# Performance work log

Hardware: AMD Instinct MI355X
Metric: run time of the kernel (lower is better)

## Reference

```python
import jax, jax.numpy as jnp
import numpy as np

FS = 48000
RIR_LENGTH = 96000
FILTER_LENGTH = 1023          # odd, so hilbert_one_sided works: N = 2*F - 1
N_FREQ = (FILTER_LENGTH + 1) // 2   # 512 rfft bins
SHARPNESS = 8.0
EPS = 1e-9
# strictly increasing fit-frequency bin indices (10 bands, like surface_freqs/dir_freqs)
FREQ_IDX = np.array([1, 2, 4, 8, 16, 32, 64, 128, 256, 480])


def get_interpolator(n_freq_target, fi):
    """numpy port of the torch get_interpolator (precomputed constant)."""
    fi = np.asarray(fi)
    r = np.zeros((len(fi), n_freq_target), np.float32)
    d = np.diff(fi)
    for i in range(len(fi)):
        if i == 0:
            r[0, :fi[1]] = np.concatenate([np.ones(fi[0]), 1 - np.arange(d[0]) / d[0]])
        elif i == len(fi) - 1:
            r[i, fi[i - 1]:] = np.concatenate([np.arange(d[i - 1]) / d[i - 1], np.ones(n_freq_target - fi[i])])
        else:
            r[i, fi[i - 1]:fi[i + 1]] = np.concatenate([np.arange(d[i - 1]) / d[i - 1], 1 - np.arange(d[i]) / d[i]])
    return r


def fibonacci_sphere(n):
    i = np.arange(n, dtype=np.float64)
    phi = np.pi * (np.sqrt(5.0) - 1.0)
    y = 1 - i / (n - 1) * 2
    rad = np.sqrt(np.maximum(1 - y * y, 0.0))
    th = phi * i
    return np.stack([np.cos(th) * rad, y, np.sin(th) * rad], -1).astype(np.float32)


def safe_log(x):
    return jnp.log(jnp.where(x <= EPS, EPS, x))


def hilbert_one_sided(x):
    """Minimum phase from log-magnitude. x: [..., F] with N = 2F-1 odd."""
    F = x.shape[-1]
    N = 2 * F - 1
    Xf = jnp.fft.irfft(x, n=N, axis=-1)
    h = jnp.concatenate([jnp.ones((1,), x.dtype),
                         2.0 * jnp.ones(((N + 1) // 2 - 1,), x.dtype),
                         jnp.zeros((N - (N + 1) // 2,), x.dtype)])
    return jnp.imag(jnp.fft.rfft(Xf * h, axis=-1))


def setup_inputs() -> dict:
    key = jax.random.key(0)
    ks = jax.random.split(key, 6)
    B, P, S, NF = 8, 4096, 16, 128
    interp = get_interpolator(N_FREQ, FREQ_IDX)  # [10, 512]
    return {
        "surface_params": jax.random.normal(ks[0], (S, len(FREQ_IDX)), jnp.float32),
        "dir_params": jax.random.normal(ks[1], (NF, len(FREQ_IDX)), jnp.float32),
        "path_dirs": jax.random.normal(ks[2], (B, P, 3), jnp.float32),
        "source_kernel": jax.random.normal(ks[3], (FILTER_LENGTH,), jnp.float32) * 0.02,
        "surf_interp": jnp.asarray(interp),
        "dir_interp": jnp.asarray(interp),
        "fib_points": jnp.asarray(fibonacci_sphere(NF)),
        "mask": jax.random.randint(ks[4], (B, P, S), 0, 3, jnp.int32),
        "delays": jax.random.randint(ks[5], (B, P), 100, RIR_LENGTH - FILTER_LENGTH - 1, jnp.int32),
    }


def reference(surface_params, dir_params, path_dirs, source_kernel,
              surf_interp, dir_interp, fib_points, mask, delays):
    B, P, _ = path_dirs.shape
    # --- per-path surface reflection log-magnitude at fit frequencies ---
    log_refl = safe_log(jax.nn.sigmoid(surface_params))            # [S, Fs]
    log_amp_s = jnp.einsum('bps,sf->bpf', mask.astype(jnp.float32), log_refl)  # [B,P,Fs]
    # --- source directivity via fibonacci-sphere softmax weighting ---
    d = path_dirs / (jnp.linalg.norm(path_dirs, axis=-1, keepdims=True) + EPS)
    w = jax.nn.softmax(SHARPNESS * jnp.einsum('bpc,nc->bpn', d, fib_points), axis=-1)  # [B,P,N]
    log_amp_d = safe_log(jnp.einsum('bpn,nf->bpf', w, jax.nn.sigmoid(dir_params)))     # [B,P,Fd]
    # --- interpolate to full frequency grid (precomputed linterp matmuls) ---
    log_amp = (jnp.einsum('bpf,fq->bpq', log_amp_s, surf_interp) +
               jnp.einsum('bpf,fq->bpq', log_amp_d, dir_interp))   # [B,P,512]
    # --- minimum phase + irfft -> per-reflection filters ---
    phase = hilbert_one_sided(log_amp)
    fr = jnp.exp(log_amp) * jnp.exp(-1j * phase)                    # complex64 [B,P,512]
    filt = jnp.fft.irfft(fr, n=FILTER_LENGTH, axis=-1)              # [B,P,1023]
    # --- 1/distance attenuation and scatter into RIR at times of arrival ---
    gains = 1.0 / jnp.maximum(delays.astype(jnp.float32) / 48.0, 1.0)  # [B,P]
    idx = delays[..., None] + jnp.arange(FILTER_LENGTH)[None, None, :]  # [B,P,L]
    rows = jnp.arange(B)[:, None, None]
    rir = jnp.zeros((B, RIR_LENGTH), jnp.float32).at[rows, idx].add(filt * gains[..., None])
    # --- convolve with learned source response kernel ('same') ---
    pad = (FILTER_LENGTH - 1) // 2
    out = jax.lax.conv_general_dilated(rir[:, None, :], source_kernel[None, None, :],
                                       window_strides=(1,), padding=[(pad, pad)],
                                       dimension_numbers=('NCH', 'OIH', 'NCH'))
    return out[:, 0, :]  # [B, RIR_LENGTH]
```

## Files before the change

kernel.cpp:

```cpp
#include <hip/hip_runtime.h>
#include <math.h>

#define N_FFTC    1023
#define NFREQ     512
#define NBANDS    10
#define NPATH     32768
#define NSURF     16
#define NDIR      128
#define RIR_LEN   96000
#define FILT_LEN  1023
#define TWO_PI_D  6.283185307179586476925286766559
#define BS        1024
#define NBINS     93

typedef _Float16 f16x8 __attribute__((ext_vector_type(8)));
typedef float    f32x4 __attribute__((ext_vector_type(4)));

#define AS1 __attribute__((address_space(1)))
#define AS3 __attribute__((address_space(3)))
__device__ __forceinline__ void gload16(const void* g, void* l) {
    __builtin_amdgcn_global_load_lds((const AS1 void*)g, (AS3 void*)l, 16, 0, 0);
}

#define WS_WT     0UL
#define WS_TWC    2097152UL
#define WS_TWS    2105344UL
#define WS_LOGR   2113536UL
#define WS_SIGD   2114560UL
#define WS_GS     2119680UL
#define WS_GD     2160640UL
#define WS_TBL    2201600UL
#define WS_WB     2283520UL
#define WS_PB     8378368UL
#define WS_A      11524096UL

__global__ void k0a_tables(const float* __restrict__ sp, const float* __restrict__ dp,
                           double* __restrict__ twc, double* __restrict__ tws,
                           float* __restrict__ logr, float* __restrict__ sigd)
{
    int idx = blockIdx.x * 256 + threadIdx.x;
    if (idx < 1023) {
        double ang = TWO_PI_D * (double)idx / 1023.0;
        twc[idx] = cos(ang);
        tws[idx] = sin(ang);
    } else if (idx >= 1024 && idx < 1024 + NSURF * NBANDS) {
        int i = idx - 1024;
        float s = 1.f / (1.f + expf(-sp[i]));
        logr[i] = logf(s <= 1e-9f ? 1e-9f : s);
    } else if (idx >= 2048 && idx < 2048 + NDIR * NBANDS) {
        int i = idx - 2048;
        sigd[i] = 1.f / (1.f + expf(-dp[i]));
    }
}

__global__ void k0b_G(const float* __restrict__ SI, const float* __restrict__ DI,
                      const double* __restrict__ twc,
                      double* __restrict__ Gs, double* __restrict__ Gd)
{
    int idx = blockIdx.x * 256 + threadIdx.x;
    if (idx >= NBANDS * NFREQ) return;
    int f = idx >> 9, n = idx & 511;
    double gs = 0.0, gd = 0.0;
    for (int m = 0; m < NFREQ; ++m) {
        double c = (m == 0) ? 1.0 : 2.0;
        double t = c * twc[(m * n) % 1023];
        gs += t * (double)SI[f * NFREQ + m];
        gd += t * (double)DI[f * NFREQ + m];
    }
    Gs[idx] = gs;
    Gd[idx] = gd;
}

__global__ void k0c_TBL(const double* __restrict__ tws,
                        const double* __restrict__ Gs, const double* __restrict__ Gd,
                        const float* __restrict__ SI, const float* __restrict__ DI,
                        float4* __restrict__ TBL)
{
    int idx = blockIdx.x * 256 + threadIdx.x;
    if (idx >= NBANDS * NFREQ) return;
    int f = idx >> 9, k = idx & 511;
    double ps = 0.0, pd_ = 0.0;
    for (int n = 1; n < 512; ++n) {
        double s = tws[(k * n) % 1023];
        ps  += s * Gs[f * NFREQ + n];
        pd_ += s * Gd[f * NFREQ + n];
    }
    double sc = -2.0 / 1023.0;
    float4 v;
    v.x = SI[idx];
    v.y = DI[idx];
    v.z = (float)(sc * ps);
    v.w = (float)(sc * pd_);
    TBL[idx] = v;
}

__global__ void k0d_W(const double* __restrict__ twc, const double* __restrict__ tws,
                      _Float16* __restrict__ WThi)
{
    int idx = blockIdx.x * 256 + threadIdx.x;
    int t = idx >> 10, k = idx & 1023;
    double v = 0.0;
    if (t < 1023) {
        if (k < 512) v = (((k == 0) ? 1.0 : 2.0) / 1023.0) * twc[(k * t) % 1023];
        else         v = (2.0 / 1023.0) * tws[((k - 512) * t) % 1023];
    }
    WThi[idx] = (_Float16)((float)(v * 16384.0));
}

__device__ __forceinline__ float wave_sum64(float v) {
#pragma unroll
    for (int m = 1; m < 64; m <<= 1) v += __shfl_xor(v, m, 64);
    return v;
}
__device__ __forceinline__ float wave_max64(float v) {
#pragma unroll
    for (int m = 1; m < 64; m <<= 1) v = fmaxf(v, __shfl_xor(v, m, 64));
    return v;
}

__global__ __launch_bounds__(256) void k1a_band(
    const float* __restrict__ path_dirs, const float* __restrict__ fib,
    const int* __restrict__ mask, const int* __restrict__ delays,
    const float* __restrict__ logr, const float* __restrict__ sigd,
    float* __restrict__ PB)
{
    int wave = threadIdx.x >> 6, lane = threadIdx.x & 63;
    int pbase = blockIdx.x * 16 + wave * 4;

    int n0 = lane, n1 = lane + 64;
    float fx0 = fib[n0 * 3], fy0 = fib[n0 * 3 + 1], fz0 = fib[n0 * 3 + 2];
    float fx1 = fib[n1 * 3], fy1 = fib[n1 * 3 + 1], fz1 = fib[n1 * 3 + 2];

    for (int pp = 0; pp < 4; ++pp) {
        int pg = pbase + pp;
        float dx = path_dirs[pg * 3 + 0], dy = path_dirs[pg * 3 + 1], dz = path_dirs[pg * 3 + 2];
        float inv = 1.f / (sqrtf(dx * dx + dy * dy + dz * dz) + 1e-9f);
        dx *= inv; dy *= inv; dz *= inv;
        float l0 = 8.f * (dx * fx0 + dy * fy0 + dz * fz0);
        float l1 = 8.f * (dx * fx1 + dy * fy1 + dz * fz1);
        float mx = wave_max64(fmaxf(l0, l1));
        float e0 = __expf(l0 - mx), e1 = __expf(l1 - mx);
        float ssum = wave_sum64(e0 + e1);
        float w0 = e0 / ssum, w1 = e1 / ssum;

        float lad[10];
#pragma unroll
        for (int f = 0; f < NBANDS; ++f) {
            float part = wave_sum64(w0 * sigd[n0 * NBANDS + f] + w1 * sigd[n1 * NBANDS + f]);
            lad[f] = __logf(part <= 1e-9f ? 1e-9f : part);
        }

        float las[10];
#pragma unroll
        for (int f = 0; f < NBANDS; ++f) las[f] = 0.f;
        const int* mrow = mask + (size_t)pg * NSURF;
#pragma unroll
        for (int s = 0; s < NSURF; ++s) {
            float mv = (float)mrow[s];
#pragma unroll
            for (int f = 0; f < NBANDS; ++f) las[f] += mv * logr[s * NBANDS + f];
        }

        int dly = delays[pg];
        float g = 1.f / fmaxf((float)dly / 48.f, 1.f);

        if (lane == 0) {
            float* pr = PB + (size_t)pg * 24;
#pragma unroll
            for (int f = 0; f < NBANDS; ++f) {
                pr[f]      = las[f];
                pr[10 + f] = lad[f];
            }
            pr[20] = g * 16384.f;
        }
    }
}

__global__ __launch_bounds__(512) void k1b_ab(
    const float4* __restrict__ TBL, const float* __restrict__ PB,
    _Float16* __restrict__ A, int chunkStart)
{
    int q = threadIdx.x;
    int pb0 = blockIdx.x * 64;

    float4 t[10];
#pragma unroll
    for (int f = 0; f < NBANDS; ++f) t[f] = TBL[f * NFREQ + q];

    for (int j = 0; j < 64; ++j) {
        const float* pr = PB + (size_t)(chunkStart + pb0 + j) * 24;
        float la = 0.f, ph = 0.f;
#pragma unroll
        for (int f = 0; f < NBANDS; ++f) {
            float ls  = pr[f];
            float ld_ = pr[10 + f];
            la += ls * t[f].x + ld_ * t[f].y;
            ph += ls * t[f].z + ld_ * t[f].w;
        }
        float M = pr[20] * __expf(la);
        float sn, cs;
        __sincosf(ph, &sn, &cs);
        _Float16* row = A + (size_t)(pb0 + j) * 1024;
        row[q]       = (_Float16)(M * cs);
        row[512 + q] = (_Float16)(M * sn);
    }
}

#define NKT 16
__global__ __launch_bounds__(512) void k2_gemm(
    const _Float16* __restrict__ A, const _Float16* __restrict__ WT,
    float* __restrict__ filt)
{
    extern __shared__ __align__(16) char smem[];

    int nwg = gridDim.x, bid = blockIdx.x;
    int swzb = (nwg & 7) ? bid : ((bid & 7) * (nwg >> 3) + (bid >> 3));
    int rowTile = swzb >> 2, colTile = swzb & 3;
    int p0 = rowTile * 256, t0 = colTile * 256;

    int tid = threadIdx.x, lane = tid & 63, wid = tid >> 6;
    int wr = wid >> 2, wc = wid & 3;
    int li = lane & 15, lg = lane >> 4, xr = li & 7;

    int srow = tid >> 3;
    int slot = (tid & 7) ^ (srow & 7);
    char* dstbase = smem + (tid & ~63) * 16;

    f32x4 acc[8][4];
#pragma unroll
    for (int i = 0; i < 8; ++i)
#pragma unroll
        for (int j = 0; j < 4; ++j) acc[i][j] = (f32x4){0.f, 0.f, 0.f, 0.f};

    auto stage = [&](int c, int hs, int kt) {
        int kk = (kt & 15) << 6;
        int off = kk + slot * 8;
        char* dst = dstbase + c * 65536 + ((hs >= 2) ? 32768 : 0) + (hs & 1) * 16384;
        if (hs < 2) {
            const _Float16* g0 = A + (size_t)(p0 + (hs & 1) * 128 + srow) * 1024 + off;
            gload16(g0, dst);
            gload16(g0 + (size_t)64 * 1024, dst + 8192);
        } else {
            const _Float16* g0 = WT + (size_t)(t0 + (hs & 1) * 128 + srow) * 1024 + off;
            gload16(g0, dst);
            gload16(g0 + (size_t)64 * 1024, dst + 8192);
        }
    };

#pragma unroll
    for (int hs = 0; hs < 4; ++hs) stage(0, hs, 0);

    int browLocal0 = (wc & 1) * 64;

    for (int kt = 0; kt < NKT; ++kt) {
        int c = kt & 1;
        int ktn = (kt + 1 < NKT) ? (kt + 1) : 0;
        const char* bufA = smem + c * 65536 + wr * 16384;
        const char* bufB = smem + c * 65536 + 32768 + (wc >> 1) * 16384;

        f16x8 bf[4][2];
#pragma unroll
        for (int ph = 0; ph < 4; ++ph) {
            stage(c ^ 1, ph, ktn);
            if (ph == 0) asm volatile("s_waitcnt vmcnt(2)" ::: "memory");
            __builtin_amdgcn_s_barrier();

            f16x8 af[2][2];
#pragma unroll
            for (int m2 = 0; m2 < 2; ++m2) {
                int row = (ph * 2 + m2) * 16 + li;
#pragma unroll
                for (int ks = 0; ks < 2; ++ks)
                    af[m2][ks] = *(const f16x8*)(bufA + row * 128 + (((ks * 4 + lg) ^ xr) << 4));
            }
            if (ph == 0) {
#pragma unroll
                for (int n = 0; n < 4; ++n) {
                    int row = browLocal0 + n * 16 + li;
#pragma unroll
                    for (int ks = 0; ks < 2; ++ks)
                        bf[n][ks] = *(const f16x8*)(bufB + row * 128 + (((ks * 4 + lg) ^ xr) << 4));
                }
            }
            __builtin_amdgcn_s_setprio(1);
#pragma unroll
            for (int m2 = 0; m2 < 2; ++m2)
#pragma unroll
                for (int n = 0; n < 4; ++n)
#pragma unroll
                    for (int ks = 0; ks < 2; ++ks)
                        acc[ph * 2 + m2][n] = __builtin_amdgcn_mfma_f32_16x16x32_f16(
                            af[m2][ks], bf[n][ks], acc[ph * 2 + m2][n], 0, 0, 0);
            __builtin_amdgcn_s_setprio(0);
            __builtin_amdgcn_s_barrier();
        }
    }

    const float dsc = 1.f / (16384.f * 16384.f);
#pragma unroll
    for (int m = 0; m < 8; ++m) {
        int prow = p0 + wr * 128 + m * 16 + lg * 4;
#pragma unroll
        for (int r = 0; r < 4; ++r) {
            float* fp = filt + (size_t)(prow + r) * 1024 + t0 + wc * 64 + li;
#pragma unroll
            for (int n = 0; n < 4; ++n)
                fp[n * 16] = acc[m][n][r] * dsc;
        }
    }
}

#define SKW(j) ((j) + ((j) >> 5))
__global__ __launch_bounds__(256) void k4_scatter(
    const float* __restrict__ filt, const int* __restrict__ delays,
    float* __restrict__ WB, int chunkStart, int m)
{
    __shared__ float win4[4][2112];
    int b = blockIdx.y, bin = blockIdx.x;
    int binStart = bin << 10;
    int wid = threadIdx.x >> 6, lane = threadIdx.x & 63;

    for (int i = lane; i < 2112; i += 64) win4[wid][i] = 0.f;

    float* w = win4[wid];
    auto ACC = [&](int off, float4 v0, float4 v1, float4 v2, float4 v3) {
        int j = off + lane * 4;
        w[SKW(j + 0)] += v0.x; w[SKW(j + 1)] += v0.y; w[SKW(j + 2)] += v0.z; w[SKW(j + 3)] += v0.w;
        j += 256;
        w[SKW(j + 0)] += v1.x; w[SKW(j + 1)] += v1.y; w[SKW(j + 2)] += v1.z; w[SKW(j + 3)] += v1.w;
        j += 256;
        w[SKW(j + 0)] += v2.x; w[SKW(j + 1)] += v2.y; w[SKW(j + 2)] += v2.z; w[SKW(j + 3)] += v2.w;
        j += 256;
        w[SKW(j + 0)] += v3.x; w[SKW(j + 1)] += v3.y; w[SKW(j + 2)] += v3.z; w[SKW(j + 3)] += v3.w;
    };

    int lo = b * 4096, hi = lo + 4096;
    if (lo < chunkStart) lo = chunkStart;
    if (hi > chunkStart + m) hi = chunkStart + m;

    for (int base = lo + wid * 64; base < hi; base += 256) {
        int p = base + lane;
        int d = (p < hi) ? delays[p] : -1;
        bool match = (d >= binStart) && (d < binStart + BS);
        unsigned long long mask = __ballot(match);
        while (mask) {
            int bit0 = __ffsll(mask) - 1; mask &= mask - 1;
            bool has2 = (mask != 0);
            int bit1 = bit0;
            if (has2) { bit1 = __ffsll(mask) - 1; mask &= mask - 1; }
            int off0 = __shfl(d, bit0) - binStart;
            int off1 = __shfl(d, bit1) - binStart;
            const float4* fr0 = (const float4*)(filt + (size_t)(base + bit0 - chunkStart) * 1024);
            const float4* fr1 = (const float4*)(filt + (size_t)(base + bit1 - chunkStart) * 1024);
            float4 a0 = fr0[lane], a1 = fr0[64 + lane], a2 = fr0[128 + lane], a3 = fr0[192 + lane];
            if (has2) {
                float4 b0 = fr1[lane], b1 = fr1[64 + lane], b2 = fr1[128 + lane], b3 = fr1[192 + lane];
                ACC(off0, a0, a1, a2, a3);
                ACC(off1, b0, b1, b2, b3);
            } else {
                ACC(off0, a0, a1, a2, a3);
            }
        }
    }
    __syncthreads();

    float* wb = WB + ((size_t)b * NBINS + bin) * 2048;
    if (chunkStart == 0) {
        for (int i = threadIdx.x; i < 2048; i += 256)
            wb[i] = win4[0][SKW(i)] + win4[1][SKW(i)] + win4[2][SKW(i)] + win4[3][SKW(i)];
    } else {
        for (int i = threadIdx.x; i < 2048; i += 256)
            wb[i] += win4[0][SKW(i)] + win4[1][SKW(i)] + win4[2][SKW(i)] + win4[3][SKW(i)];
    }
}

#define SEG 2048
#define SK(i) ((i) + ((i) >> 5))
__global__ __launch_bounds__(256) void k3_conv(
    const float* __restrict__ WB, const float* __restrict__ kern, float* __restrict__ out)
{
    __shared__ float rs[3184];
    __shared__ float ks[FILT_LEN];
    int b = blockIdx.y;
    int t0 = blockIdx.x * SEG;
    const float* wbb = WB + (size_t)b * NBINS * 2048;
    for (int i = threadIdx.x; i < FILT_LEN; i += 256) ks[i] = kern[i];
    for (int i = threadIdx.x; i < SEG + FILT_LEN - 1 + 8; i += 256) {
        int t = t0 - 511 + i;
        float v = 0.f;
        if (t >= 0 && t < RIR_LEN) {
            int bn = t >> 10, o = t & 1023;
            if (bn < NBINS) v = wbb[bn * 2048 + o];
            if (bn >= 1)    v += wbb[(bn - 1) * 2048 + o + 1024];
        }
        rs[SK(i)] = v;
    }
    __syncthreads();

    int base = threadIdx.x * 8;
    float a0 = 0.f, a1 = 0.f, a2 = 0.f, a3 = 0.f, a4 = 0.f, a5 = 0.f, a6 = 0.f, a7 = 0.f;
    float w0 = rs[SK(base + 0)], w1 = rs[SK(base + 1)], w2 = rs[SK(base + 2)], w3 = rs[SK(base + 3)];
    float w4 = rs[SK(base + 4)], w5 = rs[SK(base + 5)], w6 = rs[SK(base + 6)], w7 = rs[SK(base + 7)];
#pragma unroll 8
    for (int k = 0; k < FILT_LEN; ++k) {
        float kv = ks[k];
        a0 = fmaf(kv, w0, a0); a1 = fmaf(kv, w1, a1);
        a2 = fmaf(kv, w2, a2); a3 = fmaf(kv, w3, a3);
        a4 = fmaf(kv, w4, a4); a5 = fmaf(kv, w5, a5);
        a6 = fmaf(kv, w6, a6); a7 = fmaf(kv, w7, a7);
        w0 = w1; w1 = w2; w2 = w3; w3 = w4; w4 = w5; w5 = w6; w6 = w7;
        w7 = rs[SK(base + k + 8)];
    }
    int t = t0 + base;
    size_t ob = (size_t)b * RIR_LEN;
    if (t + 7 < RIR_LEN) {
        float4 v0 = {a0, a1, a2, a3}, v1 = {a4, a5, a6, a7};
        *(float4*)&out[ob + t]     = v0;
        *(float4*)&out[ob + t + 4] = v1;
    } else {
        float av[8] = {a0, a1, a2, a3, a4, a5, a6, a7};
        for (int j = 0; j < 8; ++j)
            if (t + j < RIR_LEN) out[ob + t + j] = av[j];
    }
}

extern "C" void kernel_launch(void* const* d_in, const int* in_sizes, int n_in,
                              void* d_out, int out_size, void* d_ws, size_t ws_size,
                              hipStream_t stream)
{
    const float* surface_params = (const float*)d_in[0];
    const float* dir_params     = (const float*)d_in[1];
    const float* path_dirs      = (const float*)d_in[2];
    const float* source_kernel  = (const float*)d_in[3];
    const float* surf_interp    = (const float*)d_in[4];
    const float* dir_interp     = (const float*)d_in[5];
    const float* fib_points     = (const float*)d_in[6];
    const int*   mask           = (const int*)d_in[7];
    const int*   delays         = (const int*)d_in[8];
    float* out = (float*)d_out;
    char*  ws  = (char*)d_ws;

    _Float16*  WT   = (_Float16*)(ws + WS_WT);
    double*    twc  = (double*)(ws + WS_TWC);
    double*    tws  = (double*)(ws + WS_TWS);
    float*     logr = (float*)(ws + WS_LOGR);
    float*     sigd = (float*)(ws + WS_SIGD);
    double*    Gs   = (double*)(ws + WS_GS);
    double*    Gd   = (double*)(ws + WS_GD);
    float4*    TBL  = (float4*)(ws + WS_TBL);
    float*     WB   = (float*)(ws + WS_WB);
    float*     PB   = (float*)(ws + WS_PB);
    _Float16*  A    = (_Float16*)(ws + WS_A);

    (void)hipFuncSetAttribute((const void*)k2_gemm,
                              hipFuncAttributeMaxDynamicSharedMemorySize, 131072);

    size_t abCap = (ws_size > WS_A) ? (ws_size - WS_A) : 0;
    long long cm = (long long)((abCap / 6144) & ~(size_t)255);
    if (cm > NPATH) cm = NPATH;
    if (cm < 256)   cm = 256;
    int chunkM = (int)cm;
    float* filt = (float*)(ws + WS_A + (size_t)chunkM * 2048);

    k0a_tables<<<16, 256, 0, stream>>>(surface_params, dir_params, twc, tws, logr, sigd);
    k0b_G     <<<20, 256, 0, stream>>>(surf_interp, dir_interp, twc, Gs, Gd);
    k0c_TBL   <<<20, 256, 0, stream>>>(tws, Gs, Gd, surf_interp, dir_interp, TBL);
    k0d_W     <<<4096, 256, 0, stream>>>(twc, tws, WT);
    k1a_band  <<<NPATH / 16, 256, 0, stream>>>(path_dirs, fib_points, mask, delays,
                                               logr, sigd, PB);

    for (int cs = 0; cs < NPATH; cs += chunkM) {
        int m = NPATH - cs;
        if (m > chunkM) m = chunkM;
        k1b_ab<<<m / 64, 512, 0, stream>>>(TBL, PB, A, cs);
        k2_gemm<<<(m / 256) * 4, 512, 131072, stream>>>(A, WT, filt);
        dim3 g4(NBINS, 8);
        k4_scatter<<<g4, 256, 0, stream>>>(filt, delays, WB, cs, m);
    }

    dim3 g3((RIR_LEN + SEG - 1) / SEG, 8);
    k3_conv<<<g3, 256, 0, stream>>>(WB, source_kernel, out);
}
```

Before: 365.3 us.

## Load GEMM B operand directly from pre-fragmented global layout, skip LDS

The DFT weight matrix is now written in a fragment-ordered layout, so each wave can load its MFMA B fragments straight from global memory (mostly L2-resident) instead of staging them through LDS. LDS use per block drops from 128KB to 64KB, which can allow two workgroups per CU and removes half of the async LDS staging traffic. The trade-off is that B fragments come from global/L2 with higher latency, issued once per k-tile without prefetch, which may stall the MFMA pipeline.

```diff
diff --git a/kernel.cpp b/kernel.cpp
--- a/kernel.cpp
+++ b/kernel.cpp
@@ -12,6 +12,7 @@
 #define TWO_PI_D  6.283185307179586476925286766559
 #define BS        1024
 #define NBINS     93
+#define NKT       16
 
 typedef _Float16 f16x8 __attribute__((ext_vector_type(8)));
 typedef float    f32x4 __attribute__((ext_vector_type(4)));
@@ -22,7 +23,7 @@
     __builtin_amdgcn_global_load_lds((const AS1 void*)g, (AS3 void*)l, 16, 0, 0);
 }
 
-#define WS_WT     0UL
+#define WS_FB     0UL
 #define WS_TWC    2097152UL
 #define WS_TWS    2105344UL
 #define WS_LOGR   2113536UL
@@ -95,7 +96,7 @@
 }
 
 __global__ void k0d_W(const double* __restrict__ twc, const double* __restrict__ tws,
-                      _Float16* __restrict__ WThi)
+                      _Float16* __restrict__ FB)
 {
     int idx = blockIdx.x * 256 + threadIdx.x;
     int t = idx >> 10, k = idx & 1023;
@@ -104,7 +105,9 @@
         if (k < 512) v = (((k == 0) ? 1.0 : 2.0) / 1023.0) * twc[(k * t) % 1023];
         else         v = (2.0 / 1023.0) * tws[((k - 512) * t) % 1023];
     }
-    WThi[idx] = (_Float16)((float)(v * 16384.0));
+    size_t off = ((size_t)((t >> 4) * NKT + (k >> 6))) * 1024
+               + ((k >> 3) & 7) * 128 + (t & 15) * 8 + (k & 7);
+    FB[off] = (_Float16)((float)(v * 16384.0));
 }
 
 __device__ __forceinline__ float wave_sum64(float v) {
@@ -206,9 +209,8 @@
     }
 }
 
-#define NKT 16
 __global__ __launch_bounds__(512) void k2_gemm(
-    const _Float16* __restrict__ A, const _Float16* __restrict__ WT,
+    const _Float16* __restrict__ A, const _Float16* __restrict__ FB,
     float* __restrict__ filt)
 {
     extern __shared__ __align__(16) char smem[];
@@ -226,6 +228,8 @@
     int slot = (tid & 7) ^ (srow & 7);
     char* dstbase = smem + (tid & ~63) * 16;
 
+    int cb = (t0 >> 4) + wc * 4;
+
     f32x4 acc[8][4];
 #pragma unroll
     for (int i = 0; i < 8; ++i)
@@ -233,35 +237,26 @@
         for (int j = 0; j < 4; ++j) acc[i][j] = (f32x4){0.f, 0.f, 0.f, 0.f};
 
     auto stage = [&](int c, int hs, int kt) {
-        int kk = (kt & 15) << 6;
-        int off = kk + slot * 8;
-        char* dst = dstbase + c * 65536 + ((hs >= 2) ? 32768 : 0) + (hs & 1) * 16384;
-        if (hs < 2) {
-            const _Float16* g0 = A + (size_t)(p0 + (hs & 1) * 128 + srow) * 1024 + off;
-            gload16(g0, dst);
-            gload16(g0 + (size_t)64 * 1024, dst + 8192);
-        } else {
-            const _Float16* g0 = WT + (size_t)(t0 + (hs & 1) * 128 + srow) * 1024 + off;
-            gload16(g0, dst);
-            gload16(g0 + (size_t)64 * 1024, dst + 8192);
-        }
+        int off = (kt << 6) + slot * 8;
+        char* dst = dstbase + c * 32768 + hs * 16384;
+        const _Float16* g0 = A + (size_t)(p0 + hs * 128 + srow) * 1024 + off;
+        gload16(g0, dst);
+        gload16(g0 + (size_t)64 * 1024, dst + 8192);
     };
 
-#pragma unroll
-    for (int hs = 0; hs < 4; ++hs) stage(0, hs, 0);
-
-    int browLocal0 = (wc & 1) * 64;
+    stage(0, 0, 0);
+    stage(0, 1, 0);
 
     for (int kt = 0; kt < NKT; ++kt) {
         int c = kt & 1;
         int ktn = (kt + 1 < NKT) ? (kt + 1) : 0;
-        const char* bufA = smem + c * 65536 + wr * 16384;
-        const char* bufB = smem + c * 65536 + 32768 + (wc >> 1) * 16384;
+        const char* bufA = smem + c * 32768 + wr * 16384;
 
         f16x8 bf[4][2];
 #pragma unroll
         for (int ph = 0; ph < 4; ++ph) {
-            stage(c ^ 1, ph, ktn);
+            if (ph == 0)      stage(c ^ 1, 0, ktn);
+            else if (ph == 2) stage(c ^ 1, 1, ktn);
             if (ph == 0) asm volatile("s_waitcnt vmcnt(2)" ::: "memory");
             __builtin_amdgcn_s_barrier();
 
@@ -275,12 +270,11 @@
             }
             if (ph == 0) {
 #pragma unroll
-                for (int n = 0; n < 4; ++n) {
-                    int row = browLocal0 + n * 16 + li;
+                for (int n = 0; n < 4; ++n)
 #pragma unroll
                     for (int ks = 0; ks < 2; ++ks)
-                        bf[n][ks] = *(const f16x8*)(bufB + row * 128 + (((ks * 4 + lg) ^ xr) << 4));
-                }
+                        bf[n][ks] = *(const f16x8*)(FB + ((size_t)(cb + n) * NKT + kt) * 1024
+                                                      + (ks * 4 + lg) * 128 + li * 8);
             }
             __builtin_amdgcn_s_setprio(1);
 #pragma unroll
@@ -440,7 +434,7 @@
     float* out = (float*)d_out;
     char*  ws  = (char*)d_ws;
 
-    _Float16*  WT   = (_Float16*)(ws + WS_WT);
+    _Float16*  FB   = (_Float16*)(ws + WS_FB);
     double*    twc  = (double*)(ws + WS_TWC);
     double*    tws  = (double*)(ws + WS_TWS);
     float*     logr = (float*)(ws + WS_LOGR);
@@ -453,7 +447,7 @@
     _Float16*  A    = (_Float16*)(ws + WS_A);
 
     (void)hipFuncSetAttribute((const void*)k2_gemm,
-                              hipFuncAttributeMaxDynamicSharedMemorySize, 131072);
+                              hipFuncAttributeMaxDynamicSharedMemorySize, 65536);
 
     size_t abCap = (ws_size > WS_A) ? (ws_size - WS_A) : 0;
     long long cm = (long long)((abCap / 6144) & ~(size_t)255);
@@ -465,7 +459,7 @@
     k0a_tables<<<16, 256, 0, stream>>>(surface_params, dir_params, twc, tws, logr, sigd);
     k0b_G     <<<20, 256, 0, stream>>>(surf_interp, dir_interp, twc, Gs, Gd);
     k0c_TBL   <<<20, 256, 0, stream>>>(tws, Gs, Gd, surf_interp, dir_interp, TBL);
-    k0d_W     <<<4096, 256, 0, stream>>>(twc, tws, WT);
+    k0d_W     <<<4096, 256, 0, stream>>>(twc, tws, FB);
     k1a_band  <<<NPATH / 16, 256, 0, stream>>>(path_dirs, fib_points, mask, delays,
                                                logr, sigd, PB);
 
@@ -473,7 +467,7 @@
         int m = NPATH - cs;
         if (m > chunkM) m = chunkM;
         k1b_ab<<<m / 64, 512, 0, stream>>>(TBL, PB, A, cs);
-        k2_gemm<<<(m / 256) * 4, 512, 131072, stream>>>(A, WT, filt);
+        k2_gemm<<<(m / 256) * 4, 512, 65536, stream>>>(A, FB, filt);
         dim3 g4(NBINS, 8);
         k4_scatter<<<g4, 256, 0, stream>>>(filt, delays, WB, cs, m);
     }
```

Result: slower. 380.7 us (+4.2%).
